# Kernel tuning notes

Measured on AMD Instinct MI355X. Metric: run time of the kernel, lower is better.

## Reference

```python
import jax, jax.numpy as jnp
import numpy as np

B, S, H, NL = 4, 1024, 400, 16
NT = 1 + 4 * NL          # O + (I,B,L,U) per label
EPS = 1e-8
NEG = -1e9


def setup_inputs() -> dict:
    key = jax.random.key(0)
    k1, k2 = jax.random.split(key, 2)
    x = jax.random.normal(k1, (B, S, H), jnp.float32)
    mask = jnp.ones((B, S), dtype=bool)
    W = jax.random.normal(k2, (H, NT), jnp.float32) * 0.02  # tag_proj weight
    b = jnp.zeros((NT,), jnp.float32)                        # tag_proj bias
    return {"x": x, "mask": mask, "W": W, "b": b}


def reference(x, mask, W, b):
    bsz, seq, _ = x.shape
    # tag projection (dropout is identity in eval)
    tag_logits = x @ W + b                       # (b, s, n_tags)
    log_marginals = jax.nn.log_softmax(tag_logits, axis=-1)  # use_crf=False path

    # per-label tags, layout per label: I, B, L, U  (tag 0 is O)
    tags = log_marginals[..., 1:].reshape(bsz, seq, NL, 4)
    I_t, B_t, L_t, U_t = tags[..., 0], tags[..., 1], tags[..., 2], tags[..., 3]

    log_is_begin = jnp.logaddexp(B_t, U_t)                 # (b, s, L)
    log_is_end = jnp.logaddexp(L_t, U_t)                   # (b, s, L)
    log_is_inside = jax.nn.logsumexp(tags, axis=-1)        # (b, s, L)

    # exclusive-prefix-padded cumsum over seq: (b, s+1, L)
    cum = jnp.concatenate(
        [jnp.zeros((bsz, 1, NL), x.dtype), jnp.cumsum(log_is_inside, axis=1)], axis=1)
    # has_no_hole[b, i, j, l] = cum[b, j+1, l] - cum[b, i, l]
    has_no_hole = cum[:, None, 1:, :] - cum[:, :-1, None, :]  # (b, s, s, L)

    span_scores = jnp.minimum(
        jnp.minimum(jnp.minimum(has_no_hole, -EPS), log_is_begin[:, :, None, :]),
        log_is_end[:, None, :, :])

    triu = jnp.triu(jnp.ones((seq, seq), dtype=bool))
    boundary_scores = jnp.where(triu[None, :, :, None], span_scores, NEG)
    return boundary_scores
```

## Files before the change

### kernel.cpp

```cpp
#include <hip/hip_runtime.h>
#include <cstddef>

#define B_   4
#define S_   1024
#define H_   400
#define NL_  16
#define NT_  65
#define EPSN (-1e-8f)
#define NEG_ (-1e9f)

__global__ __launch_bounds__(256) void k1_proj(
    const float* __restrict__ x, const float* __restrict__ W,
    const float* __restrict__ bias,
    float* __restrict__ inside, float* __restrict__ beginv,
    float* __restrict__ endv)
{
    __shared__ float xs[8 * H_];
    __shared__ float lg[8 * NT_];

    const int tid = threadIdx.x;
    const int tokBase = blockIdx.x * 8;

    {
        const float4* x4 = (const float4*)(x + (size_t)tokBase * H_);
        float4* xs4 = (float4*)xs;
        for (int idx = tid; idx < 8 * H_ / 4; idx += 256) xs4[idx] = x4[idx];
    }
    __syncthreads();

    const int t = tid >> 2, q = tid & 3;
    float acc[8];
#pragma unroll
    for (int k = 0; k < 8; ++k) acc[k] = 0.f;
    const int k0 = q * 100;
    for (int k = k0; k < k0 + 100; ++k) {
        float w = W[k * NT_ + t];
#pragma unroll
        for (int tok = 0; tok < 8; ++tok)
            acc[tok] = fmaf(xs[tok * H_ + k], w, acc[tok]);
    }
#pragma unroll
    for (int tok = 0; tok < 8; ++tok) {
        acc[tok] += __shfl_xor(acc[tok], 1);
        acc[tok] += __shfl_xor(acc[tok], 2);
    }
    if (q == 0) {
        float bt = bias[t];
#pragma unroll
        for (int tok = 0; tok < 8; ++tok) lg[tok * NT_ + t] = acc[tok] + bt;
    }
    if (tid < 4) {
        float a64[8];
#pragma unroll
        for (int k = 0; k < 8; ++k) a64[k] = 0.f;
        const int kk0 = tid * 100;
        for (int k = kk0; k < kk0 + 100; ++k) {
            float w = W[k * NT_ + 64];
#pragma unroll
            for (int tok = 0; tok < 8; ++tok)
                a64[tok] = fmaf(xs[tok * H_ + k], w, a64[tok]);
        }
#pragma unroll
        for (int tok = 0; tok < 8; ++tok) {
            a64[tok] += __shfl_xor(a64[tok], 1);
            a64[tok] += __shfl_xor(a64[tok], 2);
        }
        if (tid == 0) {
            float b64 = bias[64];
#pragma unroll
            for (int tok = 0; tok < 8; ++tok) lg[tok * NT_ + 64] = a64[tok] + b64;
        }
    }
    __syncthreads();

    const int wave = tid >> 6, lane = tid & 63;
#pragma unroll
    for (int rep = 0; rep < 2; ++rep) {
        const int tok = wave + rep * 4;
        float v   = lg[tok * NT_ + lane];
        float v64 = lg[tok * NT_ + 64];
        float m = v;
#pragma unroll
        for (int d = 32; d; d >>= 1) m = fmaxf(m, __shfl_xor(m, d));
        m = fmaxf(m, v64);
        float e = __expf(v - m);
#pragma unroll
        for (int d = 32; d; d >>= 1) e += __shfl_xor(e, d);
        e += __expf(v64 - m);
        const float logden = m + __logf(e);

        if (lane < NL_) {
            const int l = lane;
            const float vI = lg[tok * NT_ + 1 + 4 * l] - logden;
            const float vB = lg[tok * NT_ + 2 + 4 * l] - logden;
            const float vL = lg[tok * NT_ + 3 + 4 * l] - logden;
            const float vU = lg[tok * NT_ + 4 + 4 * l] - logden;
            float mb = fmaxf(vB, vU), nb = fminf(vB, vU);
            float bg = mb + log1pf(__expf(nb - mb));
            float me = fmaxf(vL, vU), ne = fminf(vL, vU);
            float en = me + log1pf(__expf(ne - me));
            float mi = fmaxf(fmaxf(vI, vB), fmaxf(vL, vU));
            float si = __expf(vI - mi) + __expf(vB - mi) +
                       __expf(vL - mi) + __expf(vU - mi);
            float ins = mi + __logf(si);

            const int gtok = tokBase + tok;
            beginv[gtok * NL_ + l] = bg;
            endv  [gtok * NL_ + l] = en;
            inside[gtok * NL_ + l] = ins;
        }
    }
}

__global__ __launch_bounds__(64) void k2_scan(
    const float* __restrict__ inside, float* __restrict__ cum)
{
    const int b = blockIdx.x >> 4, l = blockIdx.x & 15;
    const int lane = threadIdx.x;
    float p[16];
    float run = 0.f;
    const int s0 = lane * 16;
#pragma unroll
    for (int k = 0; k < 16; ++k) {
        run += inside[((b * S_) + s0 + k) * NL_ + l];
        p[k] = run;
    }
    const float tot = run;
    float sc = tot;
#pragma unroll
    for (int d = 1; d < 64; d <<= 1) {
        float o = __shfl_up(sc, d);
        if (lane >= d) sc += o;
    }
    const float excl = sc - tot;
    if (lane == 0) cum[(b * (S_ + 1)) * NL_ + l] = 0.f;
#pragma unroll
    for (int k = 0; k < 16; ++k)
        cum[((b * (S_ + 1)) + s0 + 1 + k) * NL_ + l] = excl + p[k];
}

__global__ __launch_bounds__(256) void k3_fill(
    const float* __restrict__ cum, const float* __restrict__ beginv,
    const float* __restrict__ endv, float4* __restrict__ out)
{
    const int b = blockIdx.z, i = blockIdx.y;
    const int tid = threadIdx.x;
    const int l4 = tid & 3, jj = tid >> 2;
    const int j = blockIdx.x * 64 + jj;
    const size_t outIdx = (((size_t)(b * S_ + i)) * S_ + j) * 4 + l4;

    if (blockIdx.x * 64 + 63 < i) {
        out[outIdx] = make_float4(NEG_, NEG_, NEG_, NEG_);
        return;
    }

    float4 r;
    if (i <= j) {
        const float4* cum4 = (const float4*)cum;
        const float4* bg4  = (const float4*)beginv;
        const float4* en4  = (const float4*)endv;
        float4 ci = cum4[(b * (S_ + 1) + i) * 4 + l4];
        float4 cj = cum4[(b * (S_ + 1) + j + 1) * 4 + l4];
        float4 bg = bg4[(b * S_ + i) * 4 + l4];
        float4 en = en4[(b * S_ + j) * 4 + l4];
        r.x = fminf(fminf(fminf(cj.x - ci.x, EPSN), bg.x), en.x);
        r.y = fminf(fminf(fminf(cj.y - ci.y, EPSN), bg.y), en.y);
        r.z = fminf(fminf(fminf(cj.z - ci.z, EPSN), bg.z), en.z);
        r.w = fminf(fminf(fminf(cj.w - ci.w, EPSN), bg.w), en.w);
    } else {
        r = make_float4(NEG_, NEG_, NEG_, NEG_);
    }
    out[outIdx] = r;
}

extern "C" void kernel_launch(void* const* d_in, const int* in_sizes, int n_in,
                              void* d_out, int out_size, void* d_ws, size_t ws_size,
                              hipStream_t stream) {
    const float* x    = (const float*)d_in[0];
    const float* W    = (const float*)d_in[2];
    const float* bias = (const float*)d_in[3];
    float* out = (float*)d_out;

    char* ws = (char*)d_ws;
    float* inside = (float*)(ws);
    float* beginv = (float*)(ws + 262144);
    float* endv   = (float*)(ws + 524288);
    float* cum    = (float*)(ws + 786432);

    k1_proj<<<dim3(B_ * S_ / 8), dim3(256), 0, stream>>>(x, W, bias,
                                                         inside, beginv, endv);
    k2_scan<<<dim3(B_ * NL_), dim3(64), 0, stream>>>(inside, cum);
    k3_fill<<<dim3(S_ / 64, S_, B_), dim3(256), 0, stream>>>(
        cum, beginv, endv, (float4*)out);
}
```

Measured before the change: 336.4 us.

## Restructure projection, transpose inside for scan, nontemporal wide fill stores

The projection kernel now stages the full W matrix plus 16 tokens in LDS and computes all 65 logits per token with one lane per tag, using shuffles for the per-label reductions. Inside values are written transposed so the scan can do contiguous vector loads. The fill kernel processes 256 columns per block with four stores per thread and uses nontemporal stores for the 268MB output to avoid cache pollution. The gain is meant to come mainly from a faster output write path; staging W in LDS per block adds about 104KB of LDS traffic per block and lowers occupancy in the first kernel.

After: 309.4 us. -8.0%, faster.

```diff
diff --git a/kernel.cpp b/kernel.cpp
--- a/kernel.cpp
+++ b/kernel.cpp
@@ -9,122 +9,110 @@
 #define EPSN (-1e-8f)
 #define NEG_ (-1e9f)
 
+typedef float f32x4 __attribute__((ext_vector_type(4)));
+
 __global__ __launch_bounds__(256) void k1_proj(
     const float* __restrict__ x, const float* __restrict__ W,
     const float* __restrict__ bias,
-    float* __restrict__ inside, float* __restrict__ beginv,
+    float* __restrict__ inside_t,
+    float* __restrict__ beginv,
     float* __restrict__ endv)
 {
-    __shared__ float xs[8 * H_];
-    __shared__ float lg[8 * NT_];
+    __shared__ float WL[H_ * NT_];
+    __shared__ float xs[16 * H_];
 
     const int tid = threadIdx.x;
-    const int tokBase = blockIdx.x * 8;
+    const int tokBase = blockIdx.x * 16;
 
     {
-        const float4* x4 = (const float4*)(x + (size_t)tokBase * H_);
-        float4* xs4 = (float4*)xs;
-        for (int idx = tid; idx < 8 * H_ / 4; idx += 256) xs4[idx] = x4[idx];
-    }
-    __syncthreads();
-
-    const int t = tid >> 2, q = tid & 3;
-    float acc[8];
-#pragma unroll
-    for (int k = 0; k < 8; ++k) acc[k] = 0.f;
-    const int k0 = q * 100;
-    for (int k = k0; k < k0 + 100; ++k) {
-        float w = W[k * NT_ + t];
-#pragma unroll
-        for (int tok = 0; tok < 8; ++tok)
-            acc[tok] = fmaf(xs[tok * H_ + k], w, acc[tok]);
-    }
-#pragma unroll
-    for (int tok = 0; tok < 8; ++tok) {
-        acc[tok] += __shfl_xor(acc[tok], 1);
-        acc[tok] += __shfl_xor(acc[tok], 2);
-    }
-    if (q == 0) {
-        float bt = bias[t];
-#pragma unroll
-        for (int tok = 0; tok < 8; ++tok) lg[tok * NT_ + t] = acc[tok] + bt;
-    }
-    if (tid < 4) {
-        float a64[8];
-#pragma unroll
-        for (int k = 0; k < 8; ++k) a64[k] = 0.f;
-        const int kk0 = tid * 100;
-        for (int k = kk0; k < kk0 + 100; ++k) {
-            float w = W[k * NT_ + 64];
-#pragma unroll
-            for (int tok = 0; tok < 8; ++tok)
-                a64[tok] = fmaf(xs[tok * H_ + k], w, a64[tok]);
-        }
-#pragma unroll
-        for (int tok = 0; tok < 8; ++tok) {
-            a64[tok] += __shfl_xor(a64[tok], 1);
-            a64[tok] += __shfl_xor(a64[tok], 2);
-        }
-        if (tid == 0) {
-            float b64 = bias[64];
-#pragma unroll
-            for (int tok = 0; tok < 8; ++tok) lg[tok * NT_ + 64] = a64[tok] + b64;
-        }
+        const f32x4* W4 = (const f32x4*)W;
+        f32x4* WL4 = (f32x4*)WL;
+        for (int i = tid; i < H_ * NT_ / 4; i += 256) WL4[i] = W4[i];
+        const f32x4* x4 = (const f32x4*)(x + (size_t)tokBase * H_);
+        f32x4* xs4 = (f32x4*)xs;
+        for (int i = tid; i < 16 * H_ / 4; i += 256) xs4[i] = x4[i];
     }
     __syncthreads();
 
     const int wave = tid >> 6, lane = tid & 63;
+
+    float acc[4], acc0[4];
 #pragma unroll
-    for (int rep = 0; rep < 2; ++rep) {
-        const int tok = wave + rep * 4;
-        float v   = lg[tok * NT_ + lane];
-        float v64 = lg[tok * NT_ + 64];
-        float m = v;
+    for (int r = 0; r < 4; ++r) { acc[r] = 0.f; acc0[r] = 0.f; }
+
+#pragma unroll 4
+    for (int k = 0; k < H_; ++k) {
+        const float wt = WL[k * NT_ + 1 + lane];
+        const float w0 = WL[k * NT_];
+#pragma unroll
+        for (int r = 0; r < 4; ++r) {
+            const float xv = xs[(wave * 4 + r) * H_ + k];
+            acc[r]  = fmaf(xv, wt, acc[r]);
+            acc0[r] = fmaf(xv, w0, acc0[r]);
+        }
+    }
+
+    const float bt = bias[1 + lane];
+    const float b0 = bias[0];
+    const int g = lane & ~3;
+    const int L = lane >> 2, kind = lane & 3;
+
+#pragma unroll
+    for (int r = 0; r < 4; ++r) {
+        const float lt = acc[r] + bt;
+        const float l0 = acc0[r] + b0;
+        float m = lt;
 #pragma unroll
         for (int d = 32; d; d >>= 1) m = fmaxf(m, __shfl_xor(m, d));
-        m = fmaxf(m, v64);
-        float e = __expf(v - m);
+        m = fmaxf(m, l0);
+        float e = __expf(lt - m);
 #pragma unroll
         for (int d = 32; d; d >>= 1) e += __shfl_xor(e, d);
-        e += __expf(v64 - m);
+        e += __expf(l0 - m);
         const float logden = m + __logf(e);
+        const float lm = lt - logden;
 
-        if (lane < NL_) {
-            const int l = lane;
-            const float vI = lg[tok * NT_ + 1 + 4 * l] - logden;
-            const float vB = lg[tok * NT_ + 2 + 4 * l] - logden;
-            const float vL = lg[tok * NT_ + 3 + 4 * l] - logden;
-            const float vU = lg[tok * NT_ + 4 + 4 * l] - logden;
-            float mb = fmaxf(vB, vU), nb = fminf(vB, vU);
-            float bg = mb + log1pf(__expf(nb - mb));
-            float me = fmaxf(vL, vU), ne = fminf(vL, vU);
-            float en = me + log1pf(__expf(ne - me));
-            float mi = fmaxf(fmaxf(vI, vB), fmaxf(vL, vU));
-            float si = __expf(vI - mi) + __expf(vB - mi) +
-                       __expf(vL - mi) + __expf(vU - mi);
-            float ins = mi + __logf(si);
+        const float vI = __shfl(lm, g + 0);
+        const float vB = __shfl(lm, g + 1);
+        const float vL = __shfl(lm, g + 2);
+        const float vU = __shfl(lm, g + 3);
 
-            const int gtok = tokBase + tok;
-            beginv[gtok * NL_ + l] = bg;
-            endv  [gtok * NL_ + l] = en;
-            inside[gtok * NL_ + l] = ins;
-        }
+        float mb = fmaxf(vB, vU), nb = fminf(vB, vU);
+        const float bg = mb + log1pf(__expf(nb - mb));
+        float me = fmaxf(vL, vU), ne = fminf(vL, vU);
+        const float en = me + log1pf(__expf(ne - me));
+        float mi = fmaxf(fmaxf(vI, vB), fmaxf(vL, vU));
+        const float ins = mi + __logf(__expf(vI - mi) + __expf(vB - mi) +
+                                      __expf(vL - mi) + __expf(vU - mi));
+
+        const int gtok = tokBase + wave * 4 + r;
+        const int b = gtok >> 10, s = gtok & 1023;
+        if (kind == 0) inside_t[(b * NL_ + L) * S_ + s] = ins;
+        if (kind == 1) beginv[gtok * NL_ + L] = bg;
+        if (kind == 2) endv[gtok * NL_ + L] = en;
     }
 }
 
 __global__ __launch_bounds__(64) void k2_scan(
-    const float* __restrict__ inside, float* __restrict__ cum)
+    const float* __restrict__ inside_t, float* __restrict__ cum)
 {
-    const int b = blockIdx.x >> 4, l = blockIdx.x & 15;
+    const int bl = blockIdx.x;
+    const int b = bl >> 4, l = bl & 15;
     const int lane = threadIdx.x;
+    const int s0 = lane * 16;
+
+    const f32x4* src = (const f32x4*)(inside_t + bl * S_ + s0);
+    float v[16];
+#pragma unroll
+    for (int q = 0; q < 4; ++q) {
+        f32x4 t = src[q];
+        v[q * 4 + 0] = t.x; v[q * 4 + 1] = t.y;
+        v[q * 4 + 2] = t.z; v[q * 4 + 3] = t.w;
+    }
+    float run = 0.f;
     float p[16];
-    float run = 0.f;
-    const int s0 = lane * 16;
 #pragma unroll
-    for (int k = 0; k < 16; ++k) {
-        run += inside[((b * S_) + s0 + k) * NL_ + l];
-        p[k] = run;
-    }
+    for (int k = 0; k < 16; ++k) { run += v[k]; p[k] = run; }
     const float tot = run;
     float sc = tot;
 #pragma unroll
@@ -141,36 +129,47 @@
 
 __global__ __launch_bounds__(256) void k3_fill(
     const float* __restrict__ cum, const float* __restrict__ beginv,
-    const float* __restrict__ endv, float4* __restrict__ out)
+    const float* __restrict__ endv, f32x4* __restrict__ out)
 {
     const int b = blockIdx.z, i = blockIdx.y;
     const int tid = threadIdx.x;
     const int l4 = tid & 3, jj = tid >> 2;
-    const int j = blockIdx.x * 64 + jj;
-    const size_t outIdx = (((size_t)(b * S_ + i)) * S_ + j) * 4 + l4;
+    const int jbase = blockIdx.x * 256;
+    const size_t rowBase = ((size_t)(b * S_ + i) * S_) * 4 + l4;
 
-    if (blockIdx.x * 64 + 63 < i) {
-        out[outIdx] = make_float4(NEG_, NEG_, NEG_, NEG_);
+    const f32x4 neg = { NEG_, NEG_, NEG_, NEG_ };
+
+    if (jbase + 255 < i) {
+#pragma unroll
+        for (int jr = 0; jr < 4; ++jr) {
+            const int j = jbase + jr * 64 + jj;
+            __builtin_nontemporal_store(neg, &out[rowBase + (size_t)j * 4]);
+        }
         return;
     }
 
-    float4 r;
-    if (i <= j) {
-        const float4* cum4 = (const float4*)cum;
-        const float4* bg4  = (const float4*)beginv;
-        const float4* en4  = (const float4*)endv;
-        float4 ci = cum4[(b * (S_ + 1) + i) * 4 + l4];
-        float4 cj = cum4[(b * (S_ + 1) + j + 1) * 4 + l4];
-        float4 bg = bg4[(b * S_ + i) * 4 + l4];
-        float4 en = en4[(b * S_ + j) * 4 + l4];
-        r.x = fminf(fminf(fminf(cj.x - ci.x, EPSN), bg.x), en.x);
-        r.y = fminf(fminf(fminf(cj.y - ci.y, EPSN), bg.y), en.y);
-        r.z = fminf(fminf(fminf(cj.z - ci.z, EPSN), bg.z), en.z);
-        r.w = fminf(fminf(fminf(cj.w - ci.w, EPSN), bg.w), en.w);
-    } else {
-        r = make_float4(NEG_, NEG_, NEG_, NEG_);
+    const f32x4* cum4 = (const f32x4*)cum;
+    const f32x4* bg4  = (const f32x4*)beginv;
+    const f32x4* en4  = (const f32x4*)endv;
+    const f32x4 ci = cum4[(b * (S_ + 1) + i) * 4 + l4];
+    const f32x4 bg = bg4[(b * S_ + i) * 4 + l4];
+
+#pragma unroll
+    for (int jr = 0; jr < 4; ++jr) {
+        const int j = jbase + jr * 64 + jj;
+        f32x4 r;
+        if (i <= j) {
+            const f32x4 cj = cum4[(b * (S_ + 1) + j + 1) * 4 + l4];
+            const f32x4 en = en4[(b * S_ + j) * 4 + l4];
+            r.x = fminf(fminf(fminf(cj.x - ci.x, EPSN), bg.x), en.x);
+            r.y = fminf(fminf(fminf(cj.y - ci.y, EPSN), bg.y), en.y);
+            r.z = fminf(fminf(fminf(cj.z - ci.z, EPSN), bg.z), en.z);
+            r.w = fminf(fminf(fminf(cj.w - ci.w, EPSN), bg.w), en.w);
+        } else {
+            r = neg;
+        }
+        __builtin_nontemporal_store(r, &out[rowBase + (size_t)j * 4]);
     }
-    out[outIdx] = r;
 }
 
 extern "C" void kernel_launch(void* const* d_in, const int* in_sizes, int n_in,
@@ -179,17 +178,16 @@
     const float* x    = (const float*)d_in[0];
     const float* W    = (const float*)d_in[2];
     const float* bias = (const float*)d_in[3];
-    float* out = (float*)d_out;
 
     char* ws = (char*)d_ws;
-    float* inside = (float*)(ws);
-    float* beginv = (float*)(ws + 262144);
-    float* endv   = (float*)(ws + 524288);
-    float* cum    = (float*)(ws + 786432);
+    float* inside_t = (float*)(ws);
+    float* beginv   = (float*)(ws + 262144);
+    float* endv     = (float*)(ws + 524288);
+    float* cum      = (float*)(ws + 786432);
 
-    k1_proj<<<dim3(B_ * S_ / 8), dim3(256), 0, stream>>>(x, W, bias,
-                                                         inside, beginv, endv);
-    k2_scan<<<dim3(B_ * NL_), dim3(64), 0, stream>>>(inside, cum);
-    k3_fill<<<dim3(S_ / 64, S_, B_), dim3(256), 0, stream>>>(
-        cum, beginv, endv, (float4*)out);
+    k1_proj<<<dim3(B_ * S_ / 16), dim3(256), 0, stream>>>(x, W, bias,
+                                                          inside_t, beginv, endv);
+    k2_scan<<<dim3(B_ * NL_), dim3(64), 0, stream>>>(inside_t, cum);
+    k3_fill<<<dim3(S_ / 256, S_, B_), dim3(256), 0, stream>>>(
+        cum, beginv, endv, (f32x4*)d_out);
 }
```
